# Kernel tuning notes

Measured on AMD Instinct MI355X. Metric: run time of the kernel, lower is better.

The kernel has to match this reference:

```python
import jax, jax.numpy as jnp
import numpy as np

N = 8192
D = 200


def setup_inputs() -> dict:
    key = jax.random.key(0)
    k1, k2, k3 = jax.random.split(key, 3)
    G_p = jax.random.normal(k1, (N, D), dtype=jnp.float32)
    # scale weights so exp(b + e) stays in a sane numeric range
    wb = jax.random.normal(k2, (D, 1), dtype=jnp.float32) * 0.02
    we = jax.random.normal(k3, (D, 1), dtype=jnp.float32) * 0.02
    return {"G_p": G_p, "wb": wb, "we": we, "k": 100}


def reference(G_p, wb, we, k):
    # begin / end scores: [N, 1]
    b_P = G_p @ wb
    e_P = G_p @ we
    # outer-sum span scores -> [N, N]
    numerator = jnp.exp(b_P + e_P.T)
    denominator = jnp.sum(numerator)
    candidate_probs = numerator / denominator
    upper = jnp.triu(candidate_probs)
    flat = upper.reshape(-1)
    k_max_values, flat_idx = jax.lax.top_k(flat, k)
    W = upper.shape[1]
    orig_indices = jnp.stack([flat_idx // W, flat_idx % W], axis=1)
    return orig_indices, k_max_values
```

## Files before the change

kernel.cpp:

```cpp
#include <hip/hip_runtime.h>
#include <math.h>

#define NN 8192
#define DD 200
#define KK 100

#define NBINS 1024
#define HSCALE 64.0f
#define BINW 0.015625f
#define CAND_CAP 4096
#define ROW_CAP 1024
#define COL_CAP 1024

#define OFF_B 0
#define OFF_E 8192
#define OFF_PB 16384
#define OFF_PE 18432

__global__ __launch_bounds__(256) void k_be(const float* __restrict__ G,
                                            const float* __restrict__ wb,
                                            const float* __restrict__ we,
                                            float* __restrict__ wsf) {
    __shared__ float seb[4], see[4];
    int gid = blockIdx.x * 256 + threadIdx.x;
    int row = gid >> 6;
    int lane = gid & 63;
    int wave = threadIdx.x >> 6;
    float pb = 0.f, pe = 0.f;
    if (lane < 50) {
        float4 g = ((const float4*)(G + (size_t)row * DD))[lane];
        float4 B = ((const float4*)wb)[lane];
        float4 E = ((const float4*)we)[lane];
        pb = fmaf(g.x, B.x, fmaf(g.y, B.y, fmaf(g.z, B.z, g.w * B.w)));
        pe = fmaf(g.x, E.x, fmaf(g.y, E.y, fmaf(g.z, E.z, g.w * E.w)));
    }
    for (int off = 32; off; off >>= 1) {
        pb += __shfl_xor(pb, off, 64);
        pe += __shfl_xor(pe, off, 64);
    }
    if (lane == 0) {
        wsf[OFF_B + row] = pb;
        wsf[OFF_E + row] = pe;
        seb[wave] = expf(pb);
        see[wave] = expf(pe);
    }
    __syncthreads();
    if (threadIdx.x == 0) {
        wsf[OFF_PB + blockIdx.x] = (seb[0] + seb[1]) + (seb[2] + seb[3]);
        wsf[OFF_PE + blockIdx.x] = (see[0] + see[1]) + (see[2] + see[3]);
    }
}

__global__ __launch_bounds__(1024) void k_tail(const float* __restrict__ wsf,
                                               float* __restrict__ out) {
    __shared__ float    b_s[NN];
    __shared__ float    e_s[NN];
    __shared__ float    cv[CAND_CAP];
    __shared__ unsigned ci[CAND_CAP];
    __shared__ unsigned sfx[NBINS];
    __shared__ unsigned hbl[NBINS];
    __shared__ int      rows_s[ROW_CAP];
    __shared__ float    rowb_s[ROW_CAP];
    __shared__ int      cols_s[COL_CAP];
    __shared__ float    cole_s[COL_CAP];
    __shared__ float    fr_sb[16], fr_se[16];
    __shared__ int      fr_eb[16], fr_bb[16];
    __shared__ unsigned wred[16], wtail_s[16];
    __shared__ unsigned nrows_s, ncols_s, ncand_s;
    __shared__ int      lo_s;
    __shared__ float    sums_s[4];

    int tid = threadIdx.x, wave = tid >> 6, lane = tid & 63;

    sfx[tid] = 0u; hbl[tid] = 0u;
    if (tid == 0) { nrows_s = 0u; ncols_s = 0u; ncand_s = 0u; lo_s = 0; }
    __syncthreads();

    const float4* b4 = (const float4*)(wsf + OFF_B);
    const float4* e4 = (const float4*)(wsf + OFF_E);
    for (int i = tid; i < NN / 4; i += 1024) {
        float4 bv = b4[i], ev = e4[i];
        ((float4*)b_s)[i] = bv;
        ((float4*)e_s)[i] = ev;
        int p;
        p = (int)fmaf(bv.x, HSCALE, 512.f); atomicAdd(&hbl[min(max(p,0),NBINS-1)], 1u);
        p = (int)fmaf(bv.y, HSCALE, 512.f); atomicAdd(&hbl[min(max(p,0),NBINS-1)], 1u);
        p = (int)fmaf(bv.z, HSCALE, 512.f); atomicAdd(&hbl[min(max(p,0),NBINS-1)], 1u);
        p = (int)fmaf(bv.w, HSCALE, 512.f); atomicAdd(&hbl[min(max(p,0),NBINS-1)], 1u);
        p = (int)fmaf(ev.x, HSCALE, 512.f); atomicAdd(&sfx[min(max(p,0),NBINS-1)], 1u);
        p = (int)fmaf(ev.y, HSCALE, 512.f); atomicAdd(&sfx[min(max(p,0),NBINS-1)], 1u);
        p = (int)fmaf(ev.z, HSCALE, 512.f); atomicAdd(&sfx[min(max(p,0),NBINS-1)], 1u);
        p = (int)fmaf(ev.w, HSCALE, 512.f); atomicAdd(&sfx[min(max(p,0),NBINS-1)], 1u);
    }

    float psb = wsf[OFF_PB + tid] + wsf[OFF_PB + 1024 + tid];
    float pse = wsf[OFF_PE + tid] + wsf[OFF_PE + 1024 + tid];
    for (int off = 32; off; off >>= 1) {
        psb += __shfl_xor(psb, off, 64);
        pse += __shfl_xor(pse, off, 64);
    }
    if (lane == 0) { fr_sb[wave] = psb; fr_se[wave] = pse; }
    __syncthreads();

    unsigned hb = hbl[tid];
    unsigned he = sfx[tid];
    int ebin = (he != 0u) ? tid : -1;
    int bbin = (hb != 0u) ? tid : -1;
    for (int off = 32; off; off >>= 1) {
        ebin = max(ebin, __shfl_xor(ebin, off, 64));
        bbin = max(bbin, __shfl_xor(bbin, off, 64));
    }
    if (lane == 0) { fr_eb[wave] = ebin; fr_bb[wave] = bbin; }
    unsigned v = he;
    for (int off = 1; off < 64; off <<= 1) {
        unsigned t = __shfl_down(v, off, 64);
        if (lane + off < 64) v += t;
    }
    if (lane == 0) wtail_s[wave] = v;
    __syncthreads();
    if (tid == 0) {
        float a = 0.f, b = 0.f; int c = -1, d = -1;
        for (int i = 0; i < 16; ++i) {
            a += fr_sb[i]; b += fr_se[i];
            c = max(c, fr_eb[i]); d = max(d, fr_bb[i]);
        }
        sums_s[0] = a; sums_s[1] = b;
        sums_s[2] = -8.0f + (float)(c + 1) * BINW;
        sums_s[3] = -8.0f + (float)(d + 1) * BINW;
        unsigned acc = 0, tails[16];
        for (int w = 15; w >= 0; --w) { tails[w] = acc; acc += wtail_s[w]; }
        for (int w = 0; w < 16; ++w) wtail_s[w] = tails[w];
    }
    __syncthreads();
    sfx[tid] = v + wtail_s[wave];
    __syncthreads();

    const unsigned TARGET = 2u * KK;
    int chunk = 64;
    for (int round = 0; round < 2; ++round) {
        int t = lo_s + (wave + 1) * chunk;
        unsigned c = 0;
        for (int k = 0; k < 16; ++k) {
            int p = lane + (k << 6);
            int idx = t + 512 - p;
            unsigned sv = (idx <= 0) ? sfx[0] : ((idx > NBINS - 1) ? 0u : sfx[idx]);
            c += hbl[p] * sv;
        }
        for (int off = 32; off; off >>= 1) c += __shfl_xor(c, off, 64);
        if (lane == 0) wred[wave] = c;
        __syncthreads();
        if (tid == 0) {
            for (int w = 15; w >= 0; --w)
                if (wred[w] >= TARGET) { lo_s += (w + 1) * chunk; break; }
        }
        __syncthreads();
        chunk >>= 4;
    }
    {
        int t = lo_s + wave + 1;
        if (wave < 3) {
            unsigned c = 0;
            for (int k = 0; k < 16; ++k) {
                int p = lane + (k << 6);
                int idx = t + 512 - p;
                unsigned sv = (idx <= 0) ? sfx[0] : ((idx > NBINS - 1) ? 0u : sfx[idx]);
                c += hbl[p] * sv;
            }
            for (int off = 32; off; off >>= 1) c += __shfl_xor(c, off, 64);
            if (lane == 0) wred[wave] = c;
        }
        __syncthreads();
        if (tid == 0) {
            for (int w = 2; w >= 0; --w)
                if (wred[w] >= TARGET) { lo_s += w + 1; break; }
        }
        __syncthreads();
    }
    float thr = -8.0f + (float)(lo_s - 1) * BINW;
    float emax = sums_s[2], bmax = sums_s[3];

    for (int i = tid; i < NN; i += 1024) {
        float bv = b_s[i];
        if (bv + emax >= thr) {
            unsigned pos = atomicAdd(&nrows_s, 1u);
            if (pos < ROW_CAP) { rows_s[pos] = i; rowb_s[pos] = bv; }
        }
        float ev = e_s[i];
        if (ev + bmax >= thr) {
            unsigned pos = atomicAdd(&ncols_s, 1u);
            if (pos < COL_CAP) { cols_s[pos] = i; cole_s[pos] = ev; }
        }
    }
    __syncthreads();
    int nr = (int)min(nrows_s, (unsigned)ROW_CAP);
    int nc = (int)min(ncols_s, (unsigned)COL_CAP);

    int tot = nr * nc;
    for (int idx = tid; idx < tot; idx += 1024) {
        int ri = idx / nc, cj = idx - ri * nc;
        int r = rows_s[ri], j = cols_s[cj];
        if (j < r) continue;
        float s = rowb_s[ri] + cole_s[cj];
        if (s >= thr) {
            unsigned pos = atomicAdd(&ncand_s, 1u);
            if (pos < CAND_CAP) {
                cv[pos] = s;
                ci[pos] = ((unsigned)r << 13) | (unsigned)j;
            }
        }
    }
    __syncthreads();

    unsigned M = min(ncand_s, (unsigned)CAND_CAP);
    float inv_den = 1.0f / (sums_s[0] * sums_s[1]);
    for (unsigned c2 = tid; c2 < M; c2 += 1024) {
        float vv = cv[c2];
        unsigned fi = ci[c2];
        int rank = 0;
        for (unsigned m = 0; m < M; ++m) {
            float vm = cv[m];
            rank += (vm > vv) || (vm == vv && ci[m] < fi);
        }
        if (rank < KK) {
            out[2 * rank]     = (float)(fi >> 13);
            out[2 * rank + 1] = (float)(fi & 8191u);
            out[200 + rank]   = expf(vv) * inv_den;
        }
    }
}

extern "C" void kernel_launch(void* const* d_in, const int* in_sizes, int n_in,
                              void* d_out, int out_size, void* d_ws, size_t ws_size,
                              hipStream_t stream) {
    const float* G  = (const float*)d_in[0];
    const float* wb = (const float*)d_in[1];
    const float* we = (const float*)d_in[2];
    float* out = (float*)d_out;
    float* wsf = (float*)d_ws;

    hipLaunchKernelGGL(k_be, dim3(2048), dim3(256), 0, stream, G, wb, we, wsf);
    hipLaunchKernelGGL(k_tail, dim3(1), dim3(1024), 0, stream, wsf, out);
}
```

Before: 79.22 us.

## Keep scores in registers, privatize histograms, pack rank keys into u64

```diff
diff --git a/kernel.cpp b/kernel.cpp
--- a/kernel.cpp
+++ b/kernel.cpp
@@ -51,46 +51,58 @@
     }
 }
 
+__device__ __forceinline__ unsigned ford(float f) {
+    unsigned u = __float_as_uint(f);
+    return u ^ ((u & 0x80000000u) ? 0xFFFFFFFFu : 0x80000000u);
+}
+
 __global__ __launch_bounds__(1024) void k_tail(const float* __restrict__ wsf,
                                                float* __restrict__ out) {
-    __shared__ float    b_s[NN];
-    __shared__ float    e_s[NN];
-    __shared__ float    cv[CAND_CAP];
-    __shared__ unsigned ci[CAND_CAP];
+    __shared__ unsigned long long kv[CAND_CAP];
+    __shared__ unsigned hb_par[2][NBINS];
+    __shared__ unsigned he_par[2][NBINS];
     __shared__ unsigned sfx[NBINS];
-    __shared__ unsigned hbl[NBINS];
     __shared__ int      rows_s[ROW_CAP];
     __shared__ float    rowb_s[ROW_CAP];
     __shared__ int      cols_s[COL_CAP];
     __shared__ float    cole_s[COL_CAP];
     __shared__ float    fr_sb[16], fr_se[16];
     __shared__ int      fr_eb[16], fr_bb[16];
-    __shared__ unsigned wred[16], wtail_s[16];
+    __shared__ unsigned wred[32], wtail_s[16];
     __shared__ unsigned nrows_s, ncols_s, ncand_s;
     __shared__ int      lo_s;
     __shared__ float    sums_s[4];
 
     int tid = threadIdx.x, wave = tid >> 6, lane = tid & 63;
-
-    sfx[tid] = 0u; hbl[tid] = 0u;
+    int par = wave & 1;
+
+    hb_par[0][tid] = 0u; hb_par[1][tid] = 0u;
+    he_par[0][tid] = 0u; he_par[1][tid] = 0u;
     if (tid == 0) { nrows_s = 0u; ncols_s = 0u; ncand_s = 0u; lo_s = 0; }
     __syncthreads();
 
-    const float4* b4 = (const float4*)(wsf + OFF_B);
-    const float4* e4 = (const float4*)(wsf + OFF_E);
-    for (int i = tid; i < NN / 4; i += 1024) {
-        float4 bv = b4[i], ev = e4[i];
-        ((float4*)b_s)[i] = bv;
-        ((float4*)e_s)[i] = ev;
+    float4 bv0 = ((const float4*)(wsf + OFF_B))[tid];
+    float4 ev0 = ((const float4*)(wsf + OFF_E))[tid];
+    float4 bv1 = ((const float4*)(wsf + OFF_B))[tid + 1024];
+    float4 ev1 = ((const float4*)(wsf + OFF_E))[tid + 1024];
+    {
         int p;
-        p = (int)fmaf(bv.x, HSCALE, 512.f); atomicAdd(&hbl[min(max(p,0),NBINS-1)], 1u);
-        p = (int)fmaf(bv.y, HSCALE, 512.f); atomicAdd(&hbl[min(max(p,0),NBINS-1)], 1u);
-        p = (int)fmaf(bv.z, HSCALE, 512.f); atomicAdd(&hbl[min(max(p,0),NBINS-1)], 1u);
-        p = (int)fmaf(bv.w, HSCALE, 512.f); atomicAdd(&hbl[min(max(p,0),NBINS-1)], 1u);
-        p = (int)fmaf(ev.x, HSCALE, 512.f); atomicAdd(&sfx[min(max(p,0),NBINS-1)], 1u);
-        p = (int)fmaf(ev.y, HSCALE, 512.f); atomicAdd(&sfx[min(max(p,0),NBINS-1)], 1u);
-        p = (int)fmaf(ev.z, HSCALE, 512.f); atomicAdd(&sfx[min(max(p,0),NBINS-1)], 1u);
-        p = (int)fmaf(ev.w, HSCALE, 512.f); atomicAdd(&sfx[min(max(p,0),NBINS-1)], 1u);
+        p = (int)fmaf(bv0.x, HSCALE, 512.f); atomicAdd(&hb_par[par][min(max(p,0),NBINS-1)], 1u);
+        p = (int)fmaf(bv0.y, HSCALE, 512.f); atomicAdd(&hb_par[par][min(max(p,0),NBINS-1)], 1u);
+        p = (int)fmaf(bv0.z, HSCALE, 512.f); atomicAdd(&hb_par[par][min(max(p,0),NBINS-1)], 1u);
+        p = (int)fmaf(bv0.w, HSCALE, 512.f); atomicAdd(&hb_par[par][min(max(p,0),NBINS-1)], 1u);
+        p = (int)fmaf(bv1.x, HSCALE, 512.f); atomicAdd(&hb_par[par][min(max(p,0),NBINS-1)], 1u);
+        p = (int)fmaf(bv1.y, HSCALE, 512.f); atomicAdd(&hb_par[par][min(max(p,0),NBINS-1)], 1u);
+        p = (int)fmaf(bv1.z, HSCALE, 512.f); atomicAdd(&hb_par[par][min(max(p,0),NBINS-1)], 1u);
+        p = (int)fmaf(bv1.w, HSCALE, 512.f); atomicAdd(&hb_par[par][min(max(p,0),NBINS-1)], 1u);
+        p = (int)fmaf(ev0.x, HSCALE, 512.f); atomicAdd(&he_par[par][min(max(p,0),NBINS-1)], 1u);
+        p = (int)fmaf(ev0.y, HSCALE, 512.f); atomicAdd(&he_par[par][min(max(p,0),NBINS-1)], 1u);
+        p = (int)fmaf(ev0.z, HSCALE, 512.f); atomicAdd(&he_par[par][min(max(p,0),NBINS-1)], 1u);
+        p = (int)fmaf(ev0.w, HSCALE, 512.f); atomicAdd(&he_par[par][min(max(p,0),NBINS-1)], 1u);
+        p = (int)fmaf(ev1.x, HSCALE, 512.f); atomicAdd(&he_par[par][min(max(p,0),NBINS-1)], 1u);
+        p = (int)fmaf(ev1.y, HSCALE, 512.f); atomicAdd(&he_par[par][min(max(p,0),NBINS-1)], 1u);
+        p = (int)fmaf(ev1.z, HSCALE, 512.f); atomicAdd(&he_par[par][min(max(p,0),NBINS-1)], 1u);
+        p = (int)fmaf(ev1.w, HSCALE, 512.f); atomicAdd(&he_par[par][min(max(p,0),NBINS-1)], 1u);
     }
 
     float psb = wsf[OFF_PB + tid] + wsf[OFF_PB + 1024 + tid];
@@ -102,8 +114,9 @@
     if (lane == 0) { fr_sb[wave] = psb; fr_se[wave] = pse; }
     __syncthreads();
 
-    unsigned hb = hbl[tid];
-    unsigned he = sfx[tid];
+    unsigned hb = hb_par[0][tid] + hb_par[1][tid];
+    unsigned he = he_par[0][tid] + he_par[1][tid];
+    hb_par[0][tid] = hb;
     int ebin = (he != 0u) ? tid : -1;
     int bbin = (hb != 0u) ? tid : -1;
     for (int off = 32; off; off >>= 1) {
@@ -136,60 +149,46 @@
     __syncthreads();
 
     const unsigned TARGET = 2u * KK;
-    int chunk = 64;
+    int half = lane >> 5, l5 = lane & 31;
+    int chunk = 32;
     for (int round = 0; round < 2; ++round) {
-        int t = lo_s + (wave + 1) * chunk;
+        int t = lo_s + (2 * wave + half + 1) * chunk;
         unsigned c = 0;
-        for (int k = 0; k < 16; ++k) {
-            int p = lane + (k << 6);
+        for (int k = 0; k < 32; ++k) {
+            int p = l5 + (k << 5);
             int idx = t + 512 - p;
             unsigned sv = (idx <= 0) ? sfx[0] : ((idx > NBINS - 1) ? 0u : sfx[idx]);
-            c += hbl[p] * sv;
-        }
-        for (int off = 32; off; off >>= 1) c += __shfl_xor(c, off, 64);
-        if (lane == 0) wred[wave] = c;
+            c += hb_par[0][p] * sv;
+        }
+        for (int off = 16; off; off >>= 1) c += __shfl_xor(c, off, 64);
+        if (l5 == 0) wred[2 * wave + half] = c;
         __syncthreads();
         if (tid == 0) {
-            for (int w = 15; w >= 0; --w)
+            for (int w = 31; w >= 0; --w)
                 if (wred[w] >= TARGET) { lo_s += (w + 1) * chunk; break; }
         }
         __syncthreads();
-        chunk >>= 4;
-    }
-    {
-        int t = lo_s + wave + 1;
-        if (wave < 3) {
-            unsigned c = 0;
-            for (int k = 0; k < 16; ++k) {
-                int p = lane + (k << 6);
-                int idx = t + 512 - p;
-                unsigned sv = (idx <= 0) ? sfx[0] : ((idx > NBINS - 1) ? 0u : sfx[idx]);
-                c += hbl[p] * sv;
-            }
-            for (int off = 32; off; off >>= 1) c += __shfl_xor(c, off, 64);
-            if (lane == 0) wred[wave] = c;
-        }
-        __syncthreads();
-        if (tid == 0) {
-            for (int w = 2; w >= 0; --w)
-                if (wred[w] >= TARGET) { lo_s += w + 1; break; }
-        }
-        __syncthreads();
+        chunk >>= 5;
     }
     float thr = -8.0f + (float)(lo_s - 1) * BINW;
     float emax = sums_s[2], bmax = sums_s[3];
 
-    for (int i = tid; i < NN; i += 1024) {
-        float bv = b_s[i];
-        if (bv + emax >= thr) {
-            unsigned pos = atomicAdd(&nrows_s, 1u);
-            if (pos < ROW_CAP) { rows_s[pos] = i; rowb_s[pos] = bv; }
-        }
-        float ev = e_s[i];
-        if (ev + bmax >= thr) {
-            unsigned pos = atomicAdd(&ncols_s, 1u);
-            if (pos < COL_CAP) { cols_s[pos] = i; cole_s[pos] = ev; }
-        }
+#define CANDB(val, row)                                                    \
+    if ((val) + emax >= thr) {                                             \
+        unsigned pos = atomicAdd(&nrows_s, 1u);                            \
+        if (pos < ROW_CAP) { rows_s[pos] = (row); rowb_s[pos] = (val); }   \
+    }
+#define CANDE(val, row)                                                    \
+    if ((val) + bmax >= thr) {                                             \
+        unsigned pos = atomicAdd(&ncols_s, 1u);                            \
+        if (pos < COL_CAP) { cols_s[pos] = (row); cole_s[pos] = (val); }   \
+    }
+    {
+        int r0 = 4 * tid, r1 = 4 * (tid + 1024);
+        CANDB(bv0.x, r0 + 0) CANDB(bv0.y, r0 + 1) CANDB(bv0.z, r0 + 2) CANDB(bv0.w, r0 + 3)
+        CANDB(bv1.x, r1 + 0) CANDB(bv1.y, r1 + 1) CANDB(bv1.z, r1 + 2) CANDB(bv1.w, r1 + 3)
+        CANDE(ev0.x, r0 + 0) CANDE(ev0.y, r0 + 1) CANDE(ev0.z, r0 + 2) CANDE(ev0.w, r0 + 3)
+        CANDE(ev1.x, r1 + 0) CANDE(ev1.y, r1 + 1) CANDE(ev1.z, r1 + 2) CANDE(ev1.w, r1 + 3)
     }
     __syncthreads();
     int nr = (int)min(nrows_s, (unsigned)ROW_CAP);
@@ -204,8 +203,8 @@
         if (s >= thr) {
             unsigned pos = atomicAdd(&ncand_s, 1u);
             if (pos < CAND_CAP) {
-                cv[pos] = s;
-                ci[pos] = ((unsigned)r << 13) | (unsigned)j;
+                unsigned fi = ((unsigned)r << 13) | (unsigned)j;
+                kv[pos] = ((unsigned long long)ford(s) << 32) | (unsigned)(~fi);
             }
         }
     }
@@ -214,14 +213,14 @@
     unsigned M = min(ncand_s, (unsigned)CAND_CAP);
     float inv_den = 1.0f / (sums_s[0] * sums_s[1]);
     for (unsigned c2 = tid; c2 < M; c2 += 1024) {
-        float vv = cv[c2];
-        unsigned fi = ci[c2];
+        unsigned long long kk = kv[c2];
         int rank = 0;
-        for (unsigned m = 0; m < M; ++m) {
-            float vm = cv[m];
-            rank += (vm > vv) || (vm == vv && ci[m] < fi);
-        }
+        for (unsigned m = 0; m < M; ++m) rank += (kv[m] > kk);
         if (rank < KK) {
+            unsigned hi = (unsigned)(kk >> 32);
+            unsigned fi = ~(unsigned)kk;
+            unsigned u = (hi & 0x80000000u) ? (hi ^ 0x80000000u) : ~hi;
+            float vv = __uint_as_float(u);
             out[2 * rank]     = (float)(fi >> 13);
             out[2 * rank + 1] = (float)(fi & 8191u);
             out[200 + rank]   = expf(vv) * inv_den;
```

Measured after the change: 77.67 us. No clear change (-2.0%).
